# Optimization experiments

Hardware: AMD Instinct MI355X
Metric: run time of the kernel (lower is better)

## Reference

```python
import jax, jax.numpy as jnp
import numpy as np

N = 50000       # nodes
E = 800000      # edges (before self-loops)
G = 512         # graphs in batch
IN_DIM = 128
OUT_DIM = 8
DIMS = [(IN_DIM, 32), (32, 64), (64, 128), (128, 64)]
EPS = 1e-5


def setup_inputs() -> dict:
    key = jax.random.key(0)
    ks = jax.random.split(key, 40)
    def nrm(k, shape, s=0.05):
        return jax.random.normal(k, shape, jnp.float32) * s
    inp = {}
    inp["x"] = jax.random.normal(ks[0], (N, IN_DIM), jnp.float32)
    inp["edge_index"] = jax.random.randint(ks[1], (2, E), 0, N, dtype=jnp.int32)
    inp["batch"] = jnp.sort(jax.random.randint(ks[2], (N,), 0, G, dtype=jnp.int32))
    for i, (din, dout) in enumerate(DIMS, 1):
        inp[f"W{i}"]  = nrm(ks[3 * i + 0], (din, dout))
        inp[f"as{i}"] = nrm(ks[3 * i + 1], (dout,))
        inp[f"ad{i}"] = nrm(ks[3 * i + 2], (dout,))
        inp[f"b{i}"]  = jnp.zeros((dout,), jnp.float32)
        inp[f"g{i}"]  = jnp.ones((dout,), jnp.float32)   # BN gamma
        inp[f"be{i}"] = jnp.zeros((dout,), jnp.float32)  # BN beta
    inp["Wf"] = nrm(ks[20], (64, 32)); inp["bf"] = jnp.zeros((32,), jnp.float32)
    inp["Wc"] = nrm(ks[21], (32, OUT_DIM)); inp["bc"] = jnp.zeros((OUT_DIM,), jnp.float32)
    return inp


def gat_conv(x, src, dst, W, a_s, a_d, b):
    """PyG GATConv, heads=1: linear (no bias) -> per-edge attention with
    leaky_relu(0.2) -> segment softmax over incoming edges -> scatter-add -> bias."""
    h = x @ W                                   # [N, F]
    a_src = h @ a_s                             # [N]
    a_dst = h @ a_d                             # [N]
    e = jax.nn.leaky_relu(a_src[src] + a_dst[dst], 0.2)   # [E+N]
    m = jax.ops.segment_max(e, dst, num_segments=N)
    w = jnp.exp(e - m[dst])
    denom = jax.ops.segment_sum(w, dst, num_segments=N)
    alpha = w / denom[dst]                      # self-loops guarantee denom > 0
    out = jax.ops.segment_sum(alpha[:, None] * h[src], dst, num_segments=N)
    return out + b


def batch_norm(x, g, be):
    mu = x.mean(axis=0)
    var = x.var(axis=0)                         # biased, as torch training BN
    return (x - mu) * jax.lax.rsqrt(var + EPS) * g + be


def reference(x, edge_index, batch,
              W1, as1, ad1, b1, g1, be1,
              W2, as2, ad2, b2, g2, be2,
              W3, as3, ad3, b3, g3, be3,
              W4, as4, ad4, b4, g4, be4,
              Wf, bf, Wc, bc):
    loops = jnp.arange(N, dtype=edge_index.dtype)
    src = jnp.concatenate([edge_index[0], loops])   # GATConv adds self-loops
    dst = jnp.concatenate([edge_index[1], loops])
    params = [(W1, as1, ad1, b1, g1, be1), (W2, as2, ad2, b2, g2, be2),
              (W3, as3, ad3, b3, g3, be3), (W4, as4, ad4, b4, g4, be4)]
    h = x
    for (W, a_s, a_d, b, g, be) in params:
        h = jax.nn.leaky_relu(gat_conv(h, src, dst, W, a_s, a_d, b), 0.01)
        h = batch_norm(h, g, be)
    pooled = jax.ops.segment_sum(h, batch, num_segments=G)   # global_add_pool
    z = jax.nn.leaky_relu(pooled @ Wf + bf, 0.01)
    return jax.nn.sigmoid(z @ Wc + bc)
```

## Files before the change

kernel.cpp:

```cpp
#include <hip/hip_runtime.h>
#include <math.h>

constexpr int BLK = 256;
constexpr int NBLKA = 256;
constexpr int NSH = 16;

static inline int cdiv(long a, long b) { return (int)((a + b - 1) / b); }

typedef __attribute__((ext_vector_type(8))) short short8;
typedef __attribute__((ext_vector_type(4))) float floatx4;

__device__ __forceinline__ unsigned short f2bf(float f) {
    unsigned u = __float_as_uint(f);
    unsigned r = u + 0x7fffu + ((u >> 16) & 1u);
    return (unsigned short)(r >> 16);
}
__device__ __forceinline__ float bf2f(unsigned short s) {
    return __uint_as_float(((unsigned)s) << 16);
}


__global__ void histA_k(const int* __restrict__ dst, int* __restrict__ histg,
                        int E, int nbkt, int chunk) {
    __shared__ int h[256];
    int tid = threadIdx.x, z = blockIdx.x;
    h[tid] = 0;
    __syncthreads();
    int e0 = z * chunk, e1 = min(E, e0 + chunk);
    for (int e = e0 + tid; e < e1; e += BLK) atomicAdd(&h[dst[e] >> 8], 1);
    __syncthreads();
    if (tid < nbkt) histg[z * nbkt + tid] = h[tid];
}

__global__ void blk_scan2_k(int* __restrict__ histg, int* __restrict__ bsum, int nbkt) {
    __shared__ int s[BLK];
    int t = threadIdx.x, b = blockIdx.x;
    int v = histg[t * nbkt + b];
    s[t] = v;
    __syncthreads();
    for (int o = 1; o < BLK; o <<= 1) {
        int tv = (t >= o) ? s[t - o] : 0;
        __syncthreads();
        s[t] += tv;
        __syncthreads();
    }
    histg[t * nbkt + b] = s[t] - v;
    if (t == BLK - 1) bsum[b] = s[t];
}

__global__ void scan_base_k(const int* __restrict__ bsum, int* __restrict__ bucket_base,
                            int nbkt, int E, int* __restrict__ gs, int* __restrict__ ge,
                            int G, float* __restrict__ bnstats) {
    __shared__ int s[BLK];
    int t = threadIdx.x;
    int v = (t < nbkt) ? bsum[t] : 0;
    s[t] = v;
    __syncthreads();
    for (int o = 1; o < BLK; o <<= 1) {
        int tv = (t >= o) ? s[t - o] : 0;
        __syncthreads();
        s[t] += tv;
        __syncthreads();
    }
    if (t < nbkt) bucket_base[t] = s[t] - v;
    if (t == 0) bucket_base[nbkt] = E;
    for (int i = t; i < G; i += BLK) { gs[i] = 0x7fffffff; ge[i] = -1; }
    for (int i = t; i < 4 * NSH * 256; i += BLK) bnstats[i] = 0.f;
}

__global__ void csrB_k(const unsigned* __restrict__ ebkt, const int* __restrict__ bucket_base,
                       int* __restrict__ off, unsigned short* __restrict__ csr,
                       const int* __restrict__ batch, int* __restrict__ gs,
                       int* __restrict__ ge, int N, int E, int nbkt) {
    __shared__ int dg[256];
    __shared__ int sc[256];
    int t = threadIdx.x, b = blockIdx.x;
    int n0 = b << 8;
    int cnt = min(256, N - n0);
    dg[t] = (t < cnt) ? 1 : 0;
    __syncthreads();
    int e0 = bucket_base[b], e1 = bucket_base[b + 1];
    for (int e = e0 + t; e < e1; e += BLK) atomicAdd(&dg[ebkt[e] >> 16], 1);
    __syncthreads();
    int d = dg[t];
    sc[t] = d;
    __syncthreads();
    for (int o = 1; o < BLK; o <<= 1) {
        int tv = (t >= o) ? sc[t - o] : 0;
        __syncthreads();
        sc[t] += tv;
        __syncthreads();
    }
    int loff = sc[t] - d;
    int csrbase = e0 + n0;
    if (t < cnt) {
        off[n0 + t] = csrbase + loff;
        csr[csrbase + loff] = (unsigned short)(n0 + t);
        dg[t] = loff + 1;
    }
    if (b == nbkt - 1 && t == 0) off[N] = E + N;
    int n = n0 + t;
    if (n < N) {
        int bb = batch[n];
        if (n == 0) gs[bb] = 0;
        else {
            int pb = batch[n - 1];
            if (pb != bb) { gs[bb] = n; ge[pb] = n - 1; }
        }
        if (n == N - 1) ge[bb] = N - 1;
    }
    __syncthreads();
    for (int e = e0 + t; e < e1; e += BLK) {
        unsigned w = ebkt[e];
        int pos = atomicAdd(&dg[w >> 16], 1);
        csr[csrbase + pos] = (unsigned short)(w & 0xffff);
    }
}

template <int K, int NOUT, bool AFP32, bool HASBN, bool DOTS, bool FIN>
__device__ __forceinline__ void gemm_body(int bx, const void* __restrict__ av,
                           const float* __restrict__ W,
                           const float* __restrict__ a_s, const float* __restrict__ a_d,
                           const float* __restrict__ bnst, const float* __restrict__ g_prev,
                           const float* __restrict__ be_prev, float invN,
                           const float* __restrict__ bias_l,
                           unsigned short* __restrict__ hb,
                           float* __restrict__ asrc, float* __restrict__ adst,
                           float* __restrict__ bn_out, int N) {
    constexpr int KF = K / 32;
    constexpr int NY = NOUT / 16;
    __shared__ float s_sca[K], s_scc[K];
    __shared__ float s_rs[DOTS ? K : 1], s_rd[DOTS ? K : 1], s_bd[2];
    __shared__ float sst[FIN ? 2 * NOUT : 1];
    int tid = threadIdx.x;
    if (FIN && tid < 2 * NOUT) sst[tid] = 0.f;
    if (tid < K) {
        float a = 1.f, c = 0.f;
        if (HASBN) {
            float su = 0.f, sq = 0.f;
#pragma unroll
            for (int s = 0; s < NSH; ++s) {
                su += bnst[s * 256 + tid];
                sq += bnst[s * 256 + 128 + tid];
            }
            float mu = su * invN;
            float var = sq * invN - mu * mu;
            a = g_prev[tid] * rsqrtf(var + 1e-5f);
            c = be_prev[tid] - mu * a;
        }
        s_sca[tid] = a; s_scc[tid] = c;
        if (DOTS) {
            const float* wr = W + (long)tid * NOUT;
            float rs = 0.f, rd = 0.f;
            for (int f = 0; f < NOUT; ++f) {
                float w = wr[f];
                rs += w * a_s[f];
                rd += w * a_d[f];
            }
            s_rs[tid] = rs; s_rd[tid] = rd;
        }
    }
    __syncthreads();
    if constexpr (DOTS) {
        if (tid < 2) {
            const float* r = tid ? s_rd : s_rs;
            float b = 0.f;
            for (int k = 0; k < K; ++k) b += s_scc[k] * r[k];
            s_bd[tid] = b;
        }
        __syncthreads();
    }

    int wave = tid >> 6;
    int lane = tid & 63;
    int quad = lane >> 4;
    int r16 = lane & 15;
    int blockbase = bx * 128;

    short8 afr[2][KF];
    bool valid[2];
#pragma unroll
    for (int rt = 0; rt < 2; ++rt) {
        int tilebase = blockbase + wave * 32 + rt * 16;
        valid[rt] = tilebase < N;
        if (!valid[rt]) continue;
        int arow = min(tilebase + r16, N - 1);
        if (AFP32) {
            const float* xr = (const float*)av + (long)arow * K;
#pragma unroll
            for (int kk = 0; kk < KF; ++kk) {
                float4 x0 = *(const float4*)(xr + kk * 32 + quad * 8);
                float4 x1 = *(const float4*)(xr + kk * 32 + quad * 8 + 4);
                short8 a;
                a[0] = (short)f2bf(x0.x); a[1] = (short)f2bf(x0.y);
                a[2] = (short)f2bf(x0.z); a[3] = (short)f2bf(x0.w);
                a[4] = (short)f2bf(x1.x); a[5] = (short)f2bf(x1.y);
                a[6] = (short)f2bf(x1.z); a[7] = (short)f2bf(x1.w);
                afr[rt][kk] = a;
            }
        } else {
            const unsigned short* hr = (const unsigned short*)av + (long)arow * K;
#pragma unroll
            for (int kk = 0; kk < KF; ++kk)
                afr[rt][kk] = *(const short8*)(hr + kk * 32 + quad * 8);
        }
        if constexpr (DOTS) {
            float ds = 0.f, dd = 0.f;
#pragma unroll
            for (int kk = 0; kk < KF; ++kk) {
                int kb = kk * 32 + quad * 8;
#pragma unroll
                for (int j = 0; j < 8; ++j) {
                    int k = kb + j;
                    float a = bf2f((unsigned short)afr[rt][kk][j]) * s_sca[k];
                    ds += a * s_rs[k];
                    dd += a * s_rd[k];
                }
            }
            ds += __shfl_xor(ds, 16, 64); ds += __shfl_xor(ds, 32, 64);
            dd += __shfl_xor(dd, 16, 64); dd += __shfl_xor(dd, 32, 64);
            int drow = tilebase + r16;
            if (quad == 0 && drow < N) {
                asrc[drow] = ds + s_bd[0];
                adst[drow] = dd + s_bd[1];
            }
        }
    }

#pragma unroll
    for (int y = 0; y < NY; ++y) {
        int col = y * 16 + r16;
        short8 bfr[KF];
        float biasp = 0.f;
#pragma unroll
        for (int kk = 0; kk < KF; ++kk) {
            short8 b;
#pragma unroll
            for (int j = 0; j < 8; ++j) {
                int k = kk * 32 + quad * 8 + j;
                float w = W[(long)k * NOUT + col];
                b[j] = (short)f2bf(s_sca[k] * w);
                biasp += s_scc[k] * w;
            }
            bfr[kk] = b;
        }
        biasp += __shfl_xor(biasp, 16, 64);
        biasp += __shfl_xor(biasp, 32, 64);
        if (FIN) biasp += bias_l[col];

        float sS = 0.f, sQ = 0.f;
#pragma unroll
        for (int rt = 0; rt < 2; ++rt) {
            if (!valid[rt]) continue;
            int tilebase = blockbase + wave * 32 + rt * 16;
            floatx4 acc = {0.f, 0.f, 0.f, 0.f};
#pragma unroll
            for (int kk = 0; kk < KF; ++kk)
                acc = __builtin_amdgcn_mfma_f32_16x16x32_bf16(afr[rt][kk], bfr[kk], acc, 0, 0, 0);
#pragma unroll
            for (int rr = 0; rr < 4; ++rr) {
                int srow = tilebase + quad * 4 + rr;
                if (srow < N) {
                    float v = acc[rr] + biasp;
                    if (FIN) {
                        v = v > 0.f ? v : 0.01f * v;
                        sS += v; sQ += v * v;
                    }
                    hb[(long)srow * NOUT + col] = f2bf(v);
                }
            }
        }
        if constexpr (FIN) {
            sS += __shfl_xor(sS, 16, 64); sS += __shfl_xor(sS, 32, 64);
            sQ += __shfl_xor(sQ, 16, 64); sQ += __shfl_xor(sQ, 32, 64);
            if (quad == 0) {
                atomicAdd(&sst[col], sS);
                atomicAdd(&sst[NOUT + col], sQ);
            }
        }
    }
    if constexpr (FIN) {
        __syncthreads();
        if (tid < 2 * NOUT) {
            float* base = bn_out + (bx & (NSH - 1)) * 256;
            int idx = (tid < NOUT) ? tid : (128 + tid - NOUT);
            atomicAdd(&base[idx], sst[tid]);
        }
    }
}

template <int K, int NOUT, bool AFP32, bool HASBN, bool DOTS, bool FIN>
__launch_bounds__(256)
__global__ void gemm_fused(const void* __restrict__ av, const float* __restrict__ W,
                           const float* __restrict__ a_s, const float* __restrict__ a_d,
                           const float* __restrict__ bnst, const float* __restrict__ g_prev,
                           const float* __restrict__ be_prev, float invN,
                           const float* __restrict__ bias_l,
                           unsigned short* __restrict__ hb,
                           float* __restrict__ asrc, float* __restrict__ adst,
                           float* __restrict__ bn_out, int N) {
    gemm_body<K, NOUT, AFP32, HASBN, DOTS, FIN>(blockIdx.x, av, W, a_s, a_d, bnst, g_prev,
                                                be_prev, invN, bias_l, hb, asrc, adst,
                                                bn_out, N);
}

__launch_bounds__(256)
__global__ void scatter_gemm0_k(const int* __restrict__ src, const int* __restrict__ dst,
                                const int* __restrict__ histg, const int* __restrict__ bucket_base,
                                unsigned* __restrict__ ebkt, int E, int nbkt, int chunk,
                                const float* __restrict__ x, const float* __restrict__ W0,
                                const float* __restrict__ as0, const float* __restrict__ ad0,
                                unsigned short* __restrict__ hb,
                                float* __restrict__ asrc, float* __restrict__ adst, int N) {
    if (blockIdx.x < NBLKA) {
        __shared__ int cur[256];
        int tid = threadIdx.x, z = blockIdx.x;
        if (tid < nbkt) cur[tid] = histg[z * nbkt + tid] + bucket_base[tid];
        __syncthreads();
        int e0 = z * chunk, e1 = min(E, e0 + chunk);
        for (int e = e0 + tid; e < e1; e += BLK) {
            int d = dst[e];
            int b = d >> 8;
            int pos = atomicAdd(&cur[b], 1);
            ebkt[pos] = ((unsigned)(d & 255) << 16) | (unsigned)src[e];
        }
    } else {
        gemm_body<128, 32, true, false, true, false>(blockIdx.x - NBLKA, x, W0, as0, ad0,
                                                     nullptr, nullptr, nullptr, 0.f, nullptr,
                                                     hb, asrc, adst, nullptr, N);
    }
}

template <int K, int NOUT>
__global__ void dots_k(const unsigned short* __restrict__ y, const float* __restrict__ W,
                       const float* __restrict__ a_s, const float* __restrict__ a_d,
                       const float* __restrict__ bnst, const float* __restrict__ g_prev,
                       const float* __restrict__ be_prev, float invN,
                       float* __restrict__ asrc, float* __restrict__ adst, int N) {
    __shared__ float crs[K], crd[K], s_scc[K], s_rs[K], s_rd[K], bd[2];
    int tid = threadIdx.x;
    if (tid < K) {
        float su = 0.f, sq = 0.f;
#pragma unroll
        for (int s = 0; s < NSH; ++s) {
            su += bnst[s * 256 + tid];
            sq += bnst[s * 256 + 128 + tid];
        }
        float mu = su * invN;
        float var = sq * invN - mu * mu;
        float a = g_prev[tid] * rsqrtf(var + 1e-5f);
        float c = be_prev[tid] - mu * a;
        const float* wr = W + (long)tid * NOUT;
        float rs = 0.f, rd = 0.f;
        for (int f = 0; f < NOUT; ++f) {
            float w = wr[f];
            rs += w * a_s[f];
            rd += w * a_d[f];
        }
        crs[tid] = a * rs; crd[tid] = a * rd;
        s_scc[tid] = c; s_rs[tid] = rs; s_rd[tid] = rd;
    }
    __syncthreads();
    if (tid < 2) {
        const float* r = tid ? s_rd : s_rs;
        float b = 0.f;
        for (int k = 0; k < K; ++k) b += s_scc[k] * r[k];
        bd[tid] = b;
    }
    __syncthreads();
    int n = blockIdx.x * blockDim.x + tid;
    if (n >= N) return;
    const unsigned short* yr = y + (long)n * K;
    float ds = bd[0], dd = bd[1];
#pragma unroll
    for (int kk = 0; kk < K / 8; ++kk) {
        short8 v8 = *(const short8*)(yr + kk * 8);
#pragma unroll
        for (int j = 0; j < 8; ++j) {
            float yv = bf2f((unsigned short)v8[j]);
            ds += yv * crs[kk * 8 + j];
            dd += yv * crd[kk * 8 + j];
        }
    }
    asrc[n] = ds;
    adst[n] = dd;
}

template <int DOUT, int FPL, bool FIN>
__global__ void gather_fused(const int* __restrict__ off,
                             const unsigned short* __restrict__ csr,
                             const float* __restrict__ asrc, const float* __restrict__ adst,
                             const unsigned short* __restrict__ hb,
                             const float* __restrict__ b,
                             unsigned short* __restrict__ out,
                             float* __restrict__ bn, int N) {
    constexpr int TPN = DOUT / FPL;
    constexpr int NV = FPL / 8;
    __shared__ float sst[FIN ? 2 * DOUT : 1];
    int tid = threadIdx.x;
    if constexpr (FIN) {
        if (tid < 2 * DOUT) sst[tid] = 0.f;
        __syncthreads();
    }

    int t = blockIdx.x * blockDim.x + tid;
    int d = t / TPN;
    int l = t % TPN;
    bool active = d < N;
    int lane = tid & 63;

    int p0 = 0, p1 = 0;
    float ad = 0.f;
    if (active) { p0 = off[d]; p1 = off[d + 1]; ad = adst[d]; }
    const int f0 = l * FPL;

    float acc[FPL];
#pragma unroll
    for (int i = 0; i < FPL; ++i) acc[i] = 0.f;
    float sum = 0.f;

#pragma unroll 2
    for (int p = p0; p < p1; ++p) {
        int s = csr[p];
        float e = asrc[s] + ad;
        e = e > 0.f ? e : 0.2f * e;
        float w = __expf(e);
        sum += w;
        const unsigned short* hr = hb + (long)s * DOUT + f0;
#pragma unroll
        for (int v = 0; v < NV; ++v) {
            const uint4 hv = *(const uint4*)(hr + v * 8);
            acc[v * 8 + 0] += w * bf2f((unsigned short)(hv.x & 0xffff));
            acc[v * 8 + 1] += w * bf2f((unsigned short)(hv.x >> 16));
            acc[v * 8 + 2] += w * bf2f((unsigned short)(hv.y & 0xffff));
            acc[v * 8 + 3] += w * bf2f((unsigned short)(hv.y >> 16));
            acc[v * 8 + 4] += w * bf2f((unsigned short)(hv.z & 0xffff));
            acc[v * 8 + 5] += w * bf2f((unsigned short)(hv.z >> 16));
            acc[v * 8 + 6] += w * bf2f((unsigned short)(hv.w & 0xffff));
            acc[v * 8 + 7] += w * bf2f((unsigned short)(hv.w >> 16));
        }
    }
    float inv = active ? (1.f / sum) : 0.f;

    if constexpr (!FIN) {
        if (active) {
#pragma unroll
            for (int v = 0; v < NV; ++v) {
                unsigned pk[4];
#pragma unroll
                for (int i = 0; i < 4; ++i) {
                    float v0 = acc[v * 8 + 2 * i] * inv;
                    float v1 = acc[v * 8 + 2 * i + 1] * inv;
                    pk[i] = (unsigned)f2bf(v0) | ((unsigned)f2bf(v1) << 16);
                }
                *(uint4*)(out + (long)d * DOUT + f0 + v * 8) = uint4{pk[0], pk[1], pk[2], pk[3]};
            }
        }
        return;
    } else {
#pragma unroll
        for (int v = 0; v < NV; ++v) {
            float4 b0 = *(const float4*)(b + f0 + v * 8);
            float4 b1 = *(const float4*)(b + f0 + v * 8 + 4);
            float bbv[8] = {b0.x, b0.y, b0.z, b0.w, b1.x, b1.y, b1.z, b1.w};
            unsigned pk[4];
#pragma unroll
            for (int i = 0; i < 4; ++i) {
                float v0 = acc[v * 8 + 2 * i] * inv + bbv[2 * i];
                float v1 = acc[v * 8 + 2 * i + 1] * inv + bbv[2 * i + 1];
                v0 = v0 > 0.f ? v0 : 0.01f * v0;
                v1 = v1 > 0.f ? v1 : 0.01f * v1;
                if (!active) { v0 = 0.f; v1 = 0.f; }
                acc[v * 8 + 2 * i] = v0;
                acc[v * 8 + 2 * i + 1] = v1;
                pk[i] = (unsigned)f2bf(v0) | ((unsigned)f2bf(v1) << 16);
            }
            if (active)
                *(uint4*)(out + (long)d * DOUT + f0 + v * 8) = uint4{pk[0], pk[1], pk[2], pk[3]};
        }

#pragma unroll
        for (int i = 0; i < FPL; ++i) {
            float s = acc[i];
            float q = s * s;
#pragma unroll
            for (int o = TPN; o < 64; o <<= 1) {
                s += __shfl_xor(s, o, 64);
                q += __shfl_xor(q, o, 64);
            }
            if (lane < TPN) {
                atomicAdd(&sst[f0 + i], s);
                atomicAdd(&sst[DOUT + f0 + i], q);
            }
        }
        __syncthreads();
        if (tid < 2 * DOUT) {
            float* base = bn + (blockIdx.x & (NSH - 1)) * 256;
            int idx = (tid < DOUT) ? tid : (128 + tid - DOUT);
            atomicAdd(&base[idx], sst[tid]);
        }
    }
}

__global__ void pool_head_k(const unsigned short* __restrict__ h, const int* __restrict__ gs,
                            const int* __restrict__ ge, const float* __restrict__ bnst,
                            const float* __restrict__ g4, const float* __restrict__ be4,
                            float invN, const float* __restrict__ Wf,
                            const float* __restrict__ bf, const float* __restrict__ Wc,
                            const float* __restrict__ bc, float* __restrict__ out) {
    int g = blockIdx.x;
    int t = threadIdx.x;
    int f = t & 63, sub = t >> 6;
    __shared__ float pp[4][64];
    __shared__ float p[64];
    __shared__ float z[32];
    int s0 = gs[g], s1 = ge[g];
    float acc = 0.f;
    if (s0 <= s1)
        for (int n = s0 + sub; n <= s1; n += 4) acc += bf2f(h[(long)n * 64 + f]);
    pp[sub][f] = acc;
    __syncthreads();
    if (t < 64) {
        float su = 0.f, sq = 0.f;
#pragma unroll
        for (int s = 0; s < NSH; ++s) {
            su += bnst[s * 256 + t];
            sq += bnst[s * 256 + 128 + t];
        }
        float mu = su * invN;
        float var = sq * invN - mu * mu;
        float a = g4[t] * rsqrtf(var + 1e-5f);
        float c = be4[t] - mu * a;
        float cnt = (s0 <= s1) ? (float)(s1 - s0 + 1) : 0.f;
        p[t] = a * (pp[0][t] + pp[1][t] + pp[2][t] + pp[3][t]) + cnt * c;
    }
    __syncthreads();
    if (t < 32) {
        float zacc = bf[t];
#pragma unroll
        for (int ff = 0; ff < 64; ++ff) zacc += p[ff] * Wf[ff * 32 + t];
        z[t] = zacc > 0.f ? zacc : 0.01f * zacc;
    }
    __syncthreads();
    if (t < 8) {
        float oacc = bc[t];
#pragma unroll
        for (int o = 0; o < 32; ++o) oacc += z[o] * Wc[o * 8 + t];
        out[(long)g * 8 + t] = 1.f / (1.f + __expf(-oacc));
    }
}

extern "C" void kernel_launch(void* const* d_in, const int* in_sizes, int n_in,
                              void* d_out, int out_size, void* d_ws, size_t ws_size,
                              hipStream_t stream) {
    const float* x   = (const float*)d_in[0];
    const int* ei    = (const int*)d_in[1];
    const int* batch = (const int*)d_in[2];
    const int N  = in_sizes[2];
    const int E  = in_sizes[1] / 2;
    const int ET = E + N;
    const int G  = out_size / 8;
    const int* src = ei;
    const int* dst = ei + E;

    const float *W[4], *as_[4], *ad_[4], *bb[4], *gg[4], *be_[4];
    for (int i = 0; i < 4; ++i) {
        W[i]   = (const float*)d_in[3 + 6 * i];
        as_[i] = (const float*)d_in[4 + 6 * i];
        ad_[i] = (const float*)d_in[5 + 6 * i];
        bb[i]  = (const float*)d_in[6 + 6 * i];
        gg[i]  = (const float*)d_in[7 + 6 * i];
        be_[i] = (const float*)d_in[8 + 6 * i];
    }
    const float* Wf = (const float*)d_in[27];
    const float* bfp = (const float*)d_in[28];
    const float* Wc = (const float*)d_in[29];
    const float* bc = (const float*)d_in[30];

    float* ws = (float*)d_ws;
    long off_ = 0;
    auto alloc = [&](long nelem) { float* p = ws + off_; off_ += (nelem + 3) & ~3L; return p; };
    unsigned short* h2a = (unsigned short*)alloc((long)N * 64);
    unsigned short* h2b = (unsigned short*)alloc((long)N * 64);
    unsigned short* hb  = (unsigned short*)alloc((long)N * 64);
    float* asrc     = alloc(N);
    float* adst     = alloc(N);
    float* bnstats  = alloc((long)4 * NSH * 256);
    unsigned* ebkt  = (unsigned*)alloc(E);
    int* histg      = (int*)alloc((long)NBLKA * 256);
    int* bucket_base = (int*)alloc(260);
    int* bsum       = (int*)alloc(256);
    int* off        = (int*)alloc(N + 1);
    unsigned short* csr = (unsigned short*)alloc(ET / 2 + 2);
    int* gs         = (int*)alloc(G);
    int* ge         = (int*)alloc(G);
    (void)ws_size; (void)n_in;

    const int nbkt = cdiv(N, 256);
    const int chunk = cdiv(E, NBLKA);
    const float invN = 1.f / (float)N;
    float* bn0 = bnstats + 0L * NSH * 256;
    float* bn1 = bnstats + 1L * NSH * 256;
    float* bn2 = bnstats + 2L * NSH * 256;
    float* bn3 = bnstats + 3L * NSH * 256;

    histA_k<<<NBLKA, BLK, 0, stream>>>(dst, histg, E, nbkt, chunk);
    blk_scan2_k<<<nbkt, BLK, 0, stream>>>(histg, bsum, nbkt);
    scan_base_k<<<1, BLK, 0, stream>>>(bsum, bucket_base, nbkt, E, gs, ge, G, bnstats);
    scatter_gemm0_k<<<NBLKA + cdiv(N, 128), BLK, 0, stream>>>(
        src, dst, histg, bucket_base, ebkt, E, nbkt, chunk,
        x, W[0], as_[0], ad_[0], hb, asrc, adst, N);
    csrB_k<<<nbkt, BLK, 0, stream>>>(ebkt, bucket_base, off, csr, batch, gs, ge, N, E, nbkt);

    gather_fused<32, 8, true><<<cdiv((long)N * 4, BLK), BLK, 0, stream>>>(
        off, csr, asrc, adst, hb, bb[0], h2b, bn0, N);

    dots_k<32, 64><<<cdiv(N, BLK), BLK, 0, stream>>>(
        h2b, W[1], as_[1], ad_[1], bn0, gg[0], be_[0], invN, asrc, adst, N);
    gather_fused<32, 8, false><<<cdiv((long)N * 4, BLK), BLK, 0, stream>>>(
        off, csr, asrc, adst, h2b, nullptr, hb, nullptr, N);
    gemm_fused<32, 64, false, true, false, true><<<cdiv(N, 128), 256, 0, stream>>>(
        hb, W[1], nullptr, nullptr, bn0, gg[0], be_[0], invN, bb[1], h2a,
        nullptr, nullptr, bn1, N);

    dots_k<64, 128><<<cdiv(N, BLK), BLK, 0, stream>>>(
        h2a, W[2], as_[2], ad_[2], bn1, gg[1], be_[1], invN, asrc, adst, N);
    gather_fused<64, 16, false><<<cdiv((long)N * 4, BLK), BLK, 0, stream>>>(
        off, csr, asrc, adst, h2a, nullptr, hb, nullptr, N);
    gemm_fused<64, 128, false, true, false, true><<<cdiv(N, 128), 256, 0, stream>>>(
        hb, W[2], nullptr, nullptr, bn1, gg[1], be_[1], invN, bb[2], h2b,
        nullptr, nullptr, bn2, N);

    gemm_fused<128, 64, false, true, true, false><<<cdiv(N, 128), 256, 0, stream>>>(
        h2b, W[3], as_[3], ad_[3], bn2, gg[2], be_[2], invN, nullptr, hb,
        asrc, adst, nullptr, N);
    gather_fused<64, 16, true><<<cdiv((long)N * 4, BLK), BLK, 0, stream>>>(
        off, csr, asrc, adst, hb, bb[3], h2a, bn3, N);

    pool_head_k<<<G, 256, 0, stream>>>(h2a, gs, ge, bn3, gg[3], be_[3],
                                       invN, Wf, bfp, Wc, bc, (float*)d_out);
}
```

Measured before the change: 315.4 us.

## Fuse neighbor gather with following GEMM via LDS tile and MFMA

For layers 2 and 3, the aggregate-then-transform path now runs in one kernel. Each block gathers 64 destination rows into a shared-memory bf16 tile, then multiplies that tile by the BN-folded weights with MFMA 16x16x32 instructions. It applies bias and leaky ReLU, writes the output, and accumulates the next layer's BN statistics. This removes one launch per layer and the global write and re-read of the aggregated intermediate. In exchange, every block rebuilds the folded weight fragments from global W, and the output stores are scalar.

```diff
diff --git a/kernel.cpp b/kernel.cpp
--- a/kernel.cpp
+++ b/kernel.cpp
@@ -386,29 +386,46 @@
     adst[n] = dd;
 }
 
-template <int DOUT, int FPL, bool FIN>
-__global__ void gather_fused(const int* __restrict__ off,
-                             const unsigned short* __restrict__ csr,
-                             const float* __restrict__ asrc, const float* __restrict__ adst,
-                             const unsigned short* __restrict__ hb,
-                             const float* __restrict__ b,
-                             unsigned short* __restrict__ out,
-                             float* __restrict__ bn, int N) {
-    constexpr int TPN = DOUT / FPL;
+template <int K, int NOUT>
+__launch_bounds__(256)
+__global__ void gather_gemm_k(const int* __restrict__ off,
+                              const unsigned short* __restrict__ csr,
+                              const float* __restrict__ asrc, const float* __restrict__ adst,
+                              const unsigned short* __restrict__ y,
+                              const float* __restrict__ W,
+                              const float* __restrict__ bnst, const float* __restrict__ g_prev,
+                              const float* __restrict__ be_prev, float invN,
+                              const float* __restrict__ bias_l,
+                              unsigned short* __restrict__ out_h,
+                              float* __restrict__ bn_out, int N) {
+    constexpr int FPL = K / 4;
     constexpr int NV = FPL / 8;
-    __shared__ float sst[FIN ? 2 * DOUT : 1];
+    constexpr int KF = K / 32;
+    constexpr int NY = NOUT / 16;
+    constexpr int LROW = K + 8;
+    __shared__ __align__(16) unsigned short agg[64][LROW];
+    __shared__ float s_sca[K], s_scc[K];
+    __shared__ float sst[2 * NOUT];
     int tid = threadIdx.x;
-    if constexpr (FIN) {
-        if (tid < 2 * DOUT) sst[tid] = 0.f;
-        __syncthreads();
-    }
-
-    int t = blockIdx.x * blockDim.x + tid;
-    int d = t / TPN;
-    int l = t % TPN;
+    if (tid < 2 * NOUT) sst[tid] = 0.f;
+    if (tid < K) {
+        float su = 0.f, sq = 0.f;
+#pragma unroll
+        for (int s = 0; s < NSH; ++s) {
+            su += bnst[s * 256 + tid];
+            sq += bnst[s * 256 + 128 + tid];
+        }
+        float mu = su * invN;
+        float var = sq * invN - mu * mu;
+        float a = g_prev[tid] * rsqrtf(var + 1e-5f);
+        s_sca[tid] = a;
+        s_scc[tid] = be_prev[tid] - mu * a;
+    }
+
+    int lrow = tid >> 2;
+    int l = tid & 3;
+    int d = blockIdx.x * 64 + lrow;
     bool active = d < N;
-    int lane = tid & 63;
-
     int p0 = 0, p1 = 0;
     float ad = 0.f;
     if (active) { p0 = off[d]; p1 = off[d + 1]; ad = adst[d]; }
@@ -426,7 +443,7 @@
         e = e > 0.f ? e : 0.2f * e;
         float w = __expf(e);
         sum += w;
-        const unsigned short* hr = hb + (long)s * DOUT + f0;
+        const unsigned short* hr = y + (long)s * K + f0;
 #pragma unroll
         for (int v = 0; v < NV; ++v) {
             const uint4 hv = *(const uint4*)(hr + v * 8);
@@ -442,63 +459,177 @@
     }
     float inv = active ? (1.f / sum) : 0.f;
 
-    if constexpr (!FIN) {
-        if (active) {
-#pragma unroll
-            for (int v = 0; v < NV; ++v) {
-                unsigned pk[4];
-#pragma unroll
-                for (int i = 0; i < 4; ++i) {
-                    float v0 = acc[v * 8 + 2 * i] * inv;
-                    float v1 = acc[v * 8 + 2 * i + 1] * inv;
-                    pk[i] = (unsigned)f2bf(v0) | ((unsigned)f2bf(v1) << 16);
-                }
-                *(uint4*)(out + (long)d * DOUT + f0 + v * 8) = uint4{pk[0], pk[1], pk[2], pk[3]};
-            }
-        }
-        return;
-    } else {
+#pragma unroll
+    for (int v = 0; v < NV; ++v) {
+        unsigned pk[4];
+#pragma unroll
+        for (int i = 0; i < 4; ++i) {
+            float v0 = active ? acc[v * 8 + 2 * i] * inv : 0.f;
+            float v1 = active ? acc[v * 8 + 2 * i + 1] * inv : 0.f;
+            pk[i] = (unsigned)f2bf(v0) | ((unsigned)f2bf(v1) << 16);
+        }
+        *(uint4*)&agg[lrow][f0 + v * 8] = uint4{pk[0], pk[1], pk[2], pk[3]};
+    }
+    __syncthreads();
+
+    int wave = tid >> 6;
+    int lane = tid & 63;
+    int quad = lane >> 4;
+    int r16 = lane & 15;
+    int tilebase = blockIdx.x * 64 + wave * 16;
+    int lrow2 = wave * 16 + r16;
+
+    short8 afr[KF];
+#pragma unroll
+    for (int kk = 0; kk < KF; ++kk)
+        afr[kk] = *(const short8*)&agg[lrow2][kk * 32 + quad * 8];
+
+#pragma unroll
+    for (int yy = 0; yy < NY; ++yy) {
+        int col = yy * 16 + r16;
+        short8 bfr[KF];
+        float biasp = 0.f;
+#pragma unroll
+        for (int kk = 0; kk < KF; ++kk) {
+            short8 b;
+#pragma unroll
+            for (int j = 0; j < 8; ++j) {
+                int k = kk * 32 + quad * 8 + j;
+                float w = W[(long)k * NOUT + col];
+                b[j] = (short)f2bf(s_sca[k] * w);
+                biasp += s_scc[k] * w;
+            }
+            bfr[kk] = b;
+        }
+        biasp += __shfl_xor(biasp, 16, 64);
+        biasp += __shfl_xor(biasp, 32, 64);
+        biasp += bias_l[col];
+
+        floatx4 acc4 = {0.f, 0.f, 0.f, 0.f};
+#pragma unroll
+        for (int kk = 0; kk < KF; ++kk)
+            acc4 = __builtin_amdgcn_mfma_f32_16x16x32_bf16(afr[kk], bfr[kk], acc4, 0, 0, 0);
+
+        float sS = 0.f, sQ = 0.f;
+#pragma unroll
+        for (int rr = 0; rr < 4; ++rr) {
+            int srow = tilebase + quad * 4 + rr;
+            if (srow < N) {
+                float v = acc4[rr] + biasp;
+                v = v > 0.f ? v : 0.01f * v;
+                sS += v; sQ += v * v;
+                out_h[(long)srow * NOUT + col] = f2bf(v);
+            }
+        }
+        sS += __shfl_xor(sS, 16, 64); sS += __shfl_xor(sS, 32, 64);
+        sQ += __shfl_xor(sQ, 16, 64); sQ += __shfl_xor(sQ, 32, 64);
+        if (quad == 0) {
+            atomicAdd(&sst[col], sS);
+            atomicAdd(&sst[NOUT + col], sQ);
+        }
+    }
+    __syncthreads();
+    if (tid < 2 * NOUT) {
+        float* base = bn_out + (blockIdx.x & (NSH - 1)) * 256;
+        int idx = (tid < NOUT) ? tid : (128 + tid - NOUT);
+        atomicAdd(&base[idx], sst[tid]);
+    }
+}
+
+template <int DOUT, int FPL>
+__global__ void gather_fused(const int* __restrict__ off,
+                             const unsigned short* __restrict__ csr,
+                             const float* __restrict__ asrc, const float* __restrict__ adst,
+                             const unsigned short* __restrict__ hb,
+                             const float* __restrict__ b,
+                             unsigned short* __restrict__ out,
+                             float* __restrict__ bn, int N) {
+    constexpr int TPN = DOUT / FPL;
+    constexpr int NV = FPL / 8;
+    __shared__ float sst[2 * DOUT];
+    int tid = threadIdx.x;
+    if (tid < 2 * DOUT) sst[tid] = 0.f;
+    __syncthreads();
+
+    int t = blockIdx.x * blockDim.x + tid;
+    int d = t / TPN;
+    int l = t % TPN;
+    bool active = d < N;
+    int lane = tid & 63;
+
+    int p0 = 0, p1 = 0;
+    float ad = 0.f;
+    if (active) { p0 = off[d]; p1 = off[d + 1]; ad = adst[d]; }
+    const int f0 = l * FPL;
+
+    float acc[FPL];
+#pragma unroll
+    for (int i = 0; i < FPL; ++i) acc[i] = 0.f;
+    float sum = 0.f;
+
+#pragma unroll 2
+    for (int p = p0; p < p1; ++p) {
+        int s = csr[p];
+        float e = asrc[s] + ad;
+        e = e > 0.f ? e : 0.2f * e;
+        float w = __expf(e);
+        sum += w;
+        const unsigned short* hr = hb + (long)s * DOUT + f0;
 #pragma unroll
         for (int v = 0; v < NV; ++v) {
-            float4 b0 = *(const float4*)(b + f0 + v * 8);
-            float4 b1 = *(const float4*)(b + f0 + v * 8 + 4);
-            float bbv[8] = {b0.x, b0.y, b0.z, b0.w, b1.x, b1.y, b1.z, b1.w};
-            unsigned pk[4];
-#pragma unroll
-            for (int i = 0; i < 4; ++i) {
-                float v0 = acc[v * 8 + 2 * i] * inv + bbv[2 * i];
-                float v1 = acc[v * 8 + 2 * i + 1] * inv + bbv[2 * i + 1];
-                v0 = v0 > 0.f ? v0 : 0.01f * v0;
-                v1 = v1 > 0.f ? v1 : 0.01f * v1;
-                if (!active) { v0 = 0.f; v1 = 0.f; }
-                acc[v * 8 + 2 * i] = v0;
-                acc[v * 8 + 2 * i + 1] = v1;
-                pk[i] = (unsigned)f2bf(v0) | ((unsigned)f2bf(v1) << 16);
-            }
-            if (active)
-                *(uint4*)(out + (long)d * DOUT + f0 + v * 8) = uint4{pk[0], pk[1], pk[2], pk[3]};
-        }
-
-#pragma unroll
-        for (int i = 0; i < FPL; ++i) {
-            float s = acc[i];
-            float q = s * s;
-#pragma unroll
-            for (int o = TPN; o < 64; o <<= 1) {
-                s += __shfl_xor(s, o, 64);
-                q += __shfl_xor(q, o, 64);
-            }
-            if (lane < TPN) {
-                atomicAdd(&sst[f0 + i], s);
-                atomicAdd(&sst[DOUT + f0 + i], q);
-            }
-        }
-        __syncthreads();
-        if (tid < 2 * DOUT) {
-            float* base = bn + (blockIdx.x & (NSH - 1)) * 256;
-            int idx = (tid < DOUT) ? tid : (128 + tid - DOUT);
-            atomicAdd(&base[idx], sst[tid]);
-        }
+            const uint4 hv = *(const uint4*)(hr + v * 8);
+            acc[v * 8 + 0] += w * bf2f((unsigned short)(hv.x & 0xffff));
+            acc[v * 8 + 1] += w * bf2f((unsigned short)(hv.x >> 16));
+            acc[v * 8 + 2] += w * bf2f((unsigned short)(hv.y & 0xffff));
+            acc[v * 8 + 3] += w * bf2f((unsigned short)(hv.y >> 16));
+            acc[v * 8 + 4] += w * bf2f((unsigned short)(hv.z & 0xffff));
+            acc[v * 8 + 5] += w * bf2f((unsigned short)(hv.z >> 16));
+            acc[v * 8 + 6] += w * bf2f((unsigned short)(hv.w & 0xffff));
+            acc[v * 8 + 7] += w * bf2f((unsigned short)(hv.w >> 16));
+        }
+    }
+    float inv = active ? (1.f / sum) : 0.f;
+
+#pragma unroll
+    for (int v = 0; v < NV; ++v) {
+        float4 b0 = *(const float4*)(b + f0 + v * 8);
+        float4 b1 = *(const float4*)(b + f0 + v * 8 + 4);
+        float bbv[8] = {b0.x, b0.y, b0.z, b0.w, b1.x, b1.y, b1.z, b1.w};
+        unsigned pk[4];
+#pragma unroll
+        for (int i = 0; i < 4; ++i) {
+            float v0 = acc[v * 8 + 2 * i] * inv + bbv[2 * i];
+            float v1 = acc[v * 8 + 2 * i + 1] * inv + bbv[2 * i + 1];
+            v0 = v0 > 0.f ? v0 : 0.01f * v0;
+            v1 = v1 > 0.f ? v1 : 0.01f * v1;
+            if (!active) { v0 = 0.f; v1 = 0.f; }
+            acc[v * 8 + 2 * i] = v0;
+            acc[v * 8 + 2 * i + 1] = v1;
+            pk[i] = (unsigned)f2bf(v0) | ((unsigned)f2bf(v1) << 16);
+        }
+        if (active)
+            *(uint4*)(out + (long)d * DOUT + f0 + v * 8) = uint4{pk[0], pk[1], pk[2], pk[3]};
+    }
+
+#pragma unroll
+    for (int i = 0; i < FPL; ++i) {
+        float s = acc[i];
+        float q = s * s;
+#pragma unroll
+        for (int o = TPN; o < 64; o <<= 1) {
+            s += __shfl_xor(s, o, 64);
+            q += __shfl_xor(q, o, 64);
+        }
+        if (lane < TPN) {
+            atomicAdd(&sst[f0 + i], s);
+            atomicAdd(&sst[DOUT + f0 + i], q);
+        }
+    }
+    __syncthreads();
+    if (tid < 2 * DOUT) {
+        float* base = bn + (blockIdx.x & (NSH - 1)) * 256;
+        int idx = (tid < DOUT) ? tid : (128 + tid - DOUT);
+        atomicAdd(&base[idx], sst[tid]);
     }
 }
 
@@ -612,29 +743,25 @@
         x, W[0], as_[0], ad_[0], hb, asrc, adst, N);
     csrB_k<<<nbkt, BLK, 0, stream>>>(ebkt, bucket_base, off, csr, batch, gs, ge, N, E, nbkt);
 
-    gather_fused<32, 8, true><<<cdiv((long)N * 4, BLK), BLK, 0, stream>>>(
+    gather_fused<32, 8><<<cdiv((long)N * 4, BLK), BLK, 0, stream>>>(
         off, csr, asrc, adst, hb, bb[0], h2b, bn0, N);
 
     dots_k<32, 64><<<cdiv(N, BLK), BLK, 0, stream>>>(
         h2b, W[1], as_[1], ad_[1], bn0, gg[0], be_[0], invN, asrc, adst, N);
-    gather_fused<32, 8, false><<<cdiv((long)N * 4, BLK), BLK, 0, stream>>>(
-        off, csr, asrc, adst, h2b, nullptr, hb, nullptr, N);
-    gemm_fused<32, 64, false, true, false, true><<<cdiv(N, 128), 256, 0, stream>>>(
-        hb, W[1], nullptr, nullptr, bn0, gg[0], be_[0], invN, bb[1], h2a,
-        nullptr, nullptr, bn1, N);
+    gather_gemm_k<32, 64><<<cdiv(N, 64), BLK, 0, stream>>>(
+        off, csr, asrc, adst, h2b, W[1], bn0, gg[0], be_[0], invN, bb[1],
+        h2a, bn1, N);
 
     dots_k<64, 128><<<cdiv(N, BLK), BLK, 0, stream>>>(
         h2a, W[2], as_[2], ad_[2], bn1, gg[1], be_[1], invN, asrc, adst, N);
-    gather_fused<64, 16, false><<<cdiv((long)N * 4, BLK), BLK, 0, stream>>>(
-        off, csr, asrc, adst, h2a, nullptr, hb, nullptr, N);
-    gemm_fused<64, 128, false, true, false, true><<<cdiv(N, 128), 256, 0, stream>>>(
-        hb, W[2], nullptr, nullptr, bn1, gg[1], be_[1], invN, bb[2], h2b,
-        nullptr, nullptr, bn2, N);
+    gather_gemm_k<64, 128><<<cdiv(N, 64), BLK, 0, stream>>>(
+        off, csr, asrc, adst, h2a, W[2], bn1, gg[1], be_[1], invN, bb[2],
+        h2b, bn2, N);
 
     gemm_fused<128, 64, false, true, true, false><<<cdiv(N, 128), 256, 0, stream>>>(
         h2b, W[3], as_[3], ad_[3], bn2, gg[2], be_[2], invN, nullptr, hb,
         asrc, adst, nullptr, N);
-    gather_fused<64, 16, true><<<cdiv((long)N * 4, BLK), BLK, 0, stream>>>(
+    gather_fused<64, 16><<<cdiv((long)N * 4, BLK), BLK, 0, stream>>>(
         off, csr, asrc, adst, hb, bb[3], h2a, bn3, N);
 
     pool_head_k<<<G, 256, 0, stream>>>(h2a, gs, ge, bn3, gg[3], be_[3],
```

Result: faster. 302.8 us, median of 2 (-4.0%).
